# Kernel tuning notes

Measured on AMD Instinct MI355X. Metric: run time of the kernel, lower is better.

The kernel has to match this reference:

```python
import jax, jax.numpy as jnp
import numpy as np

SEQ, DIN, DOUT, RANK = 8192, 4096, 4096, 16

def setup_inputs() -> dict:
    key = jax.random.key(0)
    ks = jax.random.split(key, 5)
    return {
        "x": jax.random.normal(ks[0], (SEQ, DIN), dtype=jnp.float32),
        "W": jax.random.normal(ks[1], (DIN, DOUT), dtype=jnp.float32) * (1.0 / np.sqrt(DIN)),
        "bias": jax.random.normal(ks[2], (DOUT,), dtype=jnp.float32),
        "A_buffer": jax.random.normal(ks[3], (DIN, RANK), dtype=jnp.float32) * (1.0 / np.sqrt(DIN)),
        "B_buffer": jax.random.normal(ks[4], (RANK, DOUT), dtype=jnp.float32),
    }

def reference(x, W, bias, A_buffer, B_buffer):
    # base linear GEMM: [seq, in] @ [in, out] -> [seq, out]
    base_output = jnp.dot(x, W)
    # LoRA path: two low-rank GEMMs fused-added onto base output
    lora_a = jnp.dot(x, A_buffer)            # [seq, rank]
    output = base_output + jnp.dot(lora_a, B_buffer)  # [seq, out]
    # module returns (output, output_bias) with bias passed through separately
    return (output, bias)
```

## Files before the change

### kernel.cpp

```cpp
#include <hip/hip_runtime.h>
#include <cstdint>
#include <cstddef>


#define SEQ  8192
#define DIN  4096
#define DOUT 4096
#define RANK 16

typedef __attribute__((ext_vector_type(8))) __bf16 bf16x8;
typedef __attribute__((ext_vector_type(4))) float f32x4;
typedef __attribute__((ext_vector_type(8))) unsigned short ushort8;

#define CAST_BLOCKS ((SEQ * DIN) / (256 * 8))
#define WEFF_BLOCKS ((DOUT / 64) * (DIN / 64))

__device__ __forceinline__ unsigned short f32_to_bf16_rne(float f) {
  union { float f; unsigned int u; } cv;
  cv.f = f;
  unsigned int u = cv.u;
  u += 0x7FFFu + ((u >> 16) & 1u);
  return (unsigned short)(u >> 16);
}

__global__ __launch_bounds__(256) void cast_kernel(
    const float* __restrict__ x, unsigned short* __restrict__ xb,
    const float* __restrict__ bias, float* __restrict__ bias_out) {
  const int tid = blockIdx.x * 256 + threadIdx.x;
  const float4* x4 = (const float4*)x;
  float4 v0 = x4[(size_t)tid * 2 + 0];
  float4 v1 = x4[(size_t)tid * 2 + 1];
  ushort8 o;
  o[0] = f32_to_bf16_rne(v0.x); o[1] = f32_to_bf16_rne(v0.y);
  o[2] = f32_to_bf16_rne(v0.z); o[3] = f32_to_bf16_rne(v0.w);
  o[4] = f32_to_bf16_rne(v1.x); o[5] = f32_to_bf16_rne(v1.y);
  o[6] = f32_to_bf16_rne(v1.z); o[7] = f32_to_bf16_rne(v1.w);
  *(ushort8*)(xb + (size_t)tid * 8) = o;
  if (tid < DOUT) bias_out[tid] = bias[tid];
}

__global__ __launch_bounds__(256) void weff_kernel(
    const float* __restrict__ W, const float* __restrict__ A,
    const float* __restrict__ B, unsigned short* __restrict__ WT) {
  __shared__ float sBf[RANK][64];
  __shared__ float sAf[64][16];
  __shared__ unsigned short sT[64][65];
  const int blk = blockIdx.x;
  const int n0 = (blk & 63) * 64;
  const int k0 = (blk >> 6) * 64;
  const int t = threadIdx.x;

  #pragma unroll
  for (int pass = 0; pass < 4; ++pass) {
    const int idx = pass * 256 + t;
    sBf[idx >> 6][idx & 63] = B[(size_t)(idx >> 6) * DOUT + n0 + (idx & 63)];
    sAf[idx >> 4][idx & 15] = A[(size_t)(k0 + (idx >> 4)) * RANK + (idx & 15)];
  }
  __syncthreads();

  const int c   = t & 63;
  const int sub = t >> 6;
  float breg[16];
  #pragma unroll
  for (int r = 0; r < 16; ++r) breg[r] = sBf[r][c];

  #pragma unroll
  for (int p = 0; p < 16; ++p) {
    const int ki = p * 4 + sub;
    const float4* ar = (const float4*)sAf[ki];
    const float4 a0 = ar[0], a1 = ar[1], a2 = ar[2], a3 = ar[3];
    float acc = W[(size_t)(k0 + ki) * DOUT + n0 + c];
    acc += a0.x * breg[0]  + a0.y * breg[1]  + a0.z * breg[2]  + a0.w * breg[3];
    acc += a1.x * breg[4]  + a1.y * breg[5]  + a1.z * breg[6]  + a1.w * breg[7];
    acc += a2.x * breg[8]  + a2.y * breg[9]  + a2.z * breg[10] + a2.w * breg[11];
    acc += a3.x * breg[12] + a3.y * breg[13] + a3.z * breg[14] + a3.w * breg[15];
    sT[ki][c] = f32_to_bf16_rne(acc);
  }
  __syncthreads();

  #pragma unroll
  for (int s = 0; s < 2; ++s) {
    const int ni = (t >> 3) + s * 32;
    const int cc = t & 7;
    ushort8 o;
    #pragma unroll
    for (int u = 0; u < 8; ++u) o[u] = sT[cc * 8 + u][ni];
    *(ushort8*)(WT + (size_t)(n0 + ni) * DIN + k0 + cc * 8) = o;
  }
}

#define BM 256
#define BN 256
#define BK 64
#define GRID_X (DOUT / BN)
#define GRID_Y (SEQ / BM)
#define NWG (GRID_X * GRID_Y)

#define BARX()   asm volatile("s_barrier" ::: "memory")
#define LGKM(n)  asm volatile("s_waitcnt lgkmcnt(" #n ")" ::: "memory")
#define VMW(n)   asm volatile("s_waitcnt vmcnt(" #n ")" ::: "memory")

#define STAGE_AH(BUF, H, KOFF)                                                 \
  __builtin_amdgcn_global_load_lds(                                            \
      (const __attribute__((address_space(1))) void*)(gA + (size_t)((H)*128 + 0)  * DIN + (KOFF)),  \
      (__attribute__((address_space(3))) void*)(sA + (BUF)*16384 + (H)*8192 + 0    + t*8), 16, 0, 0);\
  __builtin_amdgcn_global_load_lds(                                            \
      (const __attribute__((address_space(1))) void*)(gA + (size_t)((H)*128 + 64) * DIN + (KOFF)),  \
      (__attribute__((address_space(3))) void*)(sA + (BUF)*16384 + (H)*8192 + 4096 + t*8), 16, 0, 0);

#define STAGE_BH(BUF, H, KOFF)                                                 \
  __builtin_amdgcn_global_load_lds(                                            \
      (const __attribute__((address_space(1))) void*)(gB + (size_t)((H)*128 + 0)  * DIN + (KOFF)),  \
      (__attribute__((address_space(3))) void*)(sB + (BUF)*16384 + (H)*8192 + 0    + t*8), 16, 0, 0);\
  __builtin_amdgcn_global_load_lds(                                            \
      (const __attribute__((address_space(1))) void*)(gB + (size_t)((H)*128 + 64) * DIN + (KOFF)),  \
      (__attribute__((address_space(3))) void*)(sB + (BUF)*16384 + (H)*8192 + 4096 + t*8), 16, 0, 0);

#define MFMA(A, B, C) __builtin_amdgcn_mfma_f32_16x16x32_bf16(A, B, C, 0, 0, 0)

#define KTILE(CUR, KOFF1, KOFF2, S1, S234, W1, W2, W4)                         \
  {                                                                            \
    const int ab_ = (CUR) * 16384;                                             \
    const int bb_ = (CUR) * 16384;                                             \
    bf16x8 a[4][2], b01[2][2], b23[2][2];                                      \
                                     \
    _Pragma("unroll") for (int i = 0; i < 4; ++i) {                            \
      a[i][0] = *(const bf16x8*)(sA + ab_ + aoff[i] + cp0);                    \
      a[i][1] = *(const bf16x8*)(sA + ab_ + aoff[i] + cp1); }                  \
    _Pragma("unroll") for (int j = 0; j < 2; ++j) {                            \
      b01[j][0] = *(const bf16x8*)(sB + bb_ + boff[j] + cp0);                  \
      b01[j][1] = *(const bf16x8*)(sB + bb_ + boff[j] + cp1); }                \
    if (S1) { STAGE_AH((CUR) ^ 1, 1, KOFF1); }                                 \
    LGKM(8);                                                                   \
    BARX(); LGKM(0);                                                           \
    __builtin_amdgcn_s_setprio(1);                                             \
    _Pragma("unroll") for (int i = 0; i < 4; ++i)                              \
      _Pragma("unroll") for (int j = 0; j < 2; ++j) {                          \
        acc[i][j] = MFMA(a[i][0], b01[j][0], acc[i][j]);                       \
        acc[i][j] = MFMA(a[i][1], b01[j][1], acc[i][j]); }                     \
    __builtin_amdgcn_s_setprio(0);                                             \
    VMW(W1); BARX();                                                           \
                                      \
    _Pragma("unroll") for (int j = 0; j < 2; ++j) {                            \
      b23[j][0] = *(const bf16x8*)(sB + bb_ + boff[j + 2] + cp0);              \
      b23[j][1] = *(const bf16x8*)(sB + bb_ + boff[j + 2] + cp1); }            \
    if (S234) { STAGE_BH((CUR), 0, KOFF2); }                                   \
    BARX(); LGKM(0);                                                           \
    __builtin_amdgcn_s_setprio(1);                                             \
    _Pragma("unroll") for (int i = 0; i < 4; ++i)                              \
      _Pragma("unroll") for (int j = 0; j < 2; ++j) {                          \
        acc[i][j + 2] = MFMA(a[i][0], b23[j][0], acc[i][j + 2]);               \
        acc[i][j + 2] = MFMA(a[i][1], b23[j][1], acc[i][j + 2]); }             \
    __builtin_amdgcn_s_setprio(0);                                             \
    VMW(W2); BARX();                                                           \
                                      \
    _Pragma("unroll") for (int i = 0; i < 4; ++i) {                            \
      a[i][0] = *(const bf16x8*)(sA + ab_ + aoff[i + 4] + cp0);                \
      a[i][1] = *(const bf16x8*)(sA + ab_ + aoff[i + 4] + cp1); }              \
    if (S234) { STAGE_AH((CUR), 0, KOFF2); }                                   \
    BARX(); LGKM(0);                                                           \
    __builtin_amdgcn_s_setprio(1);                                             \
    _Pragma("unroll") for (int i = 0; i < 4; ++i)                              \
      _Pragma("unroll") for (int j = 0; j < 2; ++j) {                          \
        acc[i + 4][j + 2] = MFMA(a[i][0], b23[j][0], acc[i + 4][j + 2]);       \
        acc[i + 4][j + 2] = MFMA(a[i][1], b23[j][1], acc[i + 4][j + 2]); }     \
    __builtin_amdgcn_s_setprio(0);                                             \
    BARX();                                                                    \
           \
    if (S234) { STAGE_BH((CUR), 1, KOFF2); }                                   \
    __builtin_amdgcn_s_setprio(1);                                             \
    _Pragma("unroll") for (int i = 0; i < 4; ++i)                              \
      _Pragma("unroll") for (int j = 0; j < 2; ++j) {                          \
        acc[i + 4][j] = MFMA(a[i][0], b01[j][0], acc[i + 4][j]);               \
        acc[i + 4][j] = MFMA(a[i][1], b01[j][1], acc[i + 4][j]); }             \
    __builtin_amdgcn_s_setprio(0);                                             \
    VMW(W4); BARX();                                                           \
  }

__global__ __launch_bounds__(512, 2) void gemm_bt_kernel(
    const unsigned short* __restrict__ xb, const unsigned short* __restrict__ wt,
    float* __restrict__ out) {
  __shared__ unsigned short sA[2 * BM * BK];
  __shared__ unsigned short sB[2 * BN * BK];

  const int t = threadIdx.x;
  const int lane = t & 63;
  const int w    = t >> 6;
  const int wr   = w >> 2;
  const int wc   = w & 3;
  const int quad = lane >> 4;
  const int lcol = lane & 15;

  const int lid = blockIdx.y * GRID_X + blockIdx.x;
  const int swz = (lid & 7) * (NWG / 8) + (lid >> 3);
  const int n0 = (swz & (GRID_X - 1)) * BN;
  const int m0 = (swz / GRID_X) * BM;

  const int g    = (lane & 7) ^ (lane >> 3);
  const int srow = w * 8 + (lane >> 3);
  const unsigned short* gA = xb + (size_t)(m0 + srow) * DIN + g * 8;
  const unsigned short* gB = wt + (size_t)(n0 + srow) * DIN + g * 8;

  const int xorv = lcol & 7;
  const int cp0  = (quad ^ xorv) * 8;
  const int cp1  = cp0 ^ 32;
  int aoff[8], boff[4];
  #pragma unroll
  for (int i = 0; i < 8; ++i)
    aoff[i] = ((i >> 2) * 128 + wr * 64 + (i & 3) * 16 + lcol) * 64;
  #pragma unroll
  for (int j = 0; j < 4; ++j)
    boff[j] = ((j >> 1) * 128 + wc * 32 + (j & 1) * 16 + lcol) * 64;

  f32x4 acc[8][4] = {};

  STAGE_AH(0, 0, 0);  STAGE_BH(0, 0, 0);  STAGE_BH(0, 1, 0);  STAGE_AH(0, 1, 0);
  STAGE_AH(1, 0, 64); STAGE_BH(1, 0, 64); STAGE_BH(1, 1, 64); STAGE_AH(1, 1, 64);
  VMW(12);
  BARX();

  KTILE(0, 64, 128, 0, 1, 10, 10, 10);

  #pragma unroll 2
  for (int tt = 1; tt < 62; ++tt) {
    const int cur = tt & 1;
    const int koff1 = (tt + 1) * BK;
    const int koff2 = (tt + 2) * BK;
    KTILE(cur, koff1, koff2, 1, 1, 10, 10, 10);
  }

  KTILE(0, 63 * BK, 0, 1, 0, 10, 8, 6);
  KTILE(1, 0, 0, 0, 0, 2, 0, 0);

  #pragma unroll
  for (int i = 0; i < 8; ++i) {
    const int rb = m0 + (i >> 2) * 128 + wr * 64 + (i & 3) * 16 + quad * 4;
    #pragma unroll
    for (int j = 0; j < 4; ++j) {
      const int cb = n0 + (j >> 1) * 128 + wc * 32 + (j & 1) * 16 + lcol;
      #pragma unroll
      for (int r = 0; r < 4; ++r)
        out[(size_t)(rb + r) * DOUT + cb] = acc[i][j][r];
    }
  }
}

extern "C" void kernel_launch(void* const* d_in, const int* in_sizes, int n_in,
                              void* d_out, int out_size, void* d_ws, size_t ws_size,
                              hipStream_t stream) {
  const float* x    = (const float*)d_in[0];
  const float* W    = (const float*)d_in[1];
  const float* bias = (const float*)d_in[2];
  const float* A    = (const float*)d_in[3];
  const float* B    = (const float*)d_in[4];
  float* out      = (float*)d_out;
  float* bias_out = out + (size_t)SEQ * DOUT;

  unsigned short* xb = (unsigned short*)d_ws;
  unsigned short* wt = xb + (size_t)SEQ * DIN;

  cast_kernel<<<CAST_BLOCKS, 256, 0, stream>>>(x, xb, bias, bias_out);
  weff_kernel<<<WEFF_BLOCKS, 256, 0, stream>>>(W, A, B, wt);
  gemm_bt_kernel<<<dim3(GRID_X, GRID_Y), 512, 0, stream>>>(xb, wt, out);
}
```

Measured before the change: 518.3 us.

## Restructure K-tile pipeline to drop barriers and LDS waitcnts, reorder staging

Reworks the per-K-tile schedule of the bf16 GEMM: removes the explicit lgkmcnt waits and one barrier per phase, moves the B-half-0 prefetch next to the A-half-0 prefetch, and passes per-phase vmcnt waits as macro arguments. The prologue now issues seven half-tile loads in B-first order and the loop starts at tile 0 instead of peeling it. The aim is fewer barrier stalls and better overlap of global-to-LDS loads with MFMA. Removing the lgkmcnt waits relies on the compiler inserting them for the LDS reads, and the changed vmcnt counts risk races if they are miscounted.

```diff
diff --git a/kernel.cpp b/kernel.cpp
--- a/kernel.cpp
+++ b/kernel.cpp
@@ -97,7 +97,6 @@
 #define NWG (GRID_X * GRID_Y)
 
 #define BARX()   asm volatile("s_barrier" ::: "memory")
-#define LGKM(n)  asm volatile("s_waitcnt lgkmcnt(" #n ")" ::: "memory")
 #define VMW(n)   asm volatile("s_waitcnt vmcnt(" #n ")" ::: "memory")
 
 #define STAGE_AH(BUF, H, KOFF)                                                 \
@@ -118,63 +117,57 @@
 
 #define MFMA(A, B, C) __builtin_amdgcn_mfma_f32_16x16x32_bf16(A, B, C, 0, 0, 0)
 
-#define KTILE(CUR, KOFF1, KOFF2, S1, S234, W1, W2, W4)                         \
+#define KTILE(CUR, KOFF1, KOFF2, S1, S34, W1, W2, W4)                          \
   {                                                                            \
     const int ab_ = (CUR) * 16384;                                             \
-    const int bb_ = (CUR) * 16384;                                             \
     bf16x8 a[4][2], b01[2][2], b23[2][2];                                      \
-                                     \
+                                                            \
     _Pragma("unroll") for (int i = 0; i < 4; ++i) {                            \
       a[i][0] = *(const bf16x8*)(sA + ab_ + aoff[i] + cp0);                    \
       a[i][1] = *(const bf16x8*)(sA + ab_ + aoff[i] + cp1); }                  \
     _Pragma("unroll") for (int j = 0; j < 2; ++j) {                            \
-      b01[j][0] = *(const bf16x8*)(sB + bb_ + boff[j] + cp0);                  \
-      b01[j][1] = *(const bf16x8*)(sB + bb_ + boff[j] + cp1); }                \
+      b01[j][0] = *(const bf16x8*)(sB + ab_ + boff[j] + cp0);                  \
+      b01[j][1] = *(const bf16x8*)(sB + ab_ + boff[j] + cp1); }                \
     if (S1) { STAGE_AH((CUR) ^ 1, 1, KOFF1); }                                 \
-    LGKM(8);                                                                   \
-    BARX(); LGKM(0);                                                           \
+    W1; BARX();                                                                \
     __builtin_amdgcn_s_setprio(1);                                             \
     _Pragma("unroll") for (int i = 0; i < 4; ++i)                              \
       _Pragma("unroll") for (int j = 0; j < 2; ++j) {                          \
         acc[i][j] = MFMA(a[i][0], b01[j][0], acc[i][j]);                       \
         acc[i][j] = MFMA(a[i][1], b01[j][1], acc[i][j]); }                     \
     __builtin_amdgcn_s_setprio(0);                                             \
-    VMW(W1); BARX();                                                           \
-                                      \
+                                                            \
     _Pragma("unroll") for (int j = 0; j < 2; ++j) {                            \
-      b23[j][0] = *(const bf16x8*)(sB + bb_ + boff[j + 2] + cp0);              \
-      b23[j][1] = *(const bf16x8*)(sB + bb_ + boff[j + 2] + cp1); }            \
-    if (S234) { STAGE_BH((CUR), 0, KOFF2); }                                   \
-    BARX(); LGKM(0);                                                           \
+      b23[j][0] = *(const bf16x8*)(sB + ab_ + boff[j + 2] + cp0);              \
+      b23[j][1] = *(const bf16x8*)(sB + ab_ + boff[j + 2] + cp1); }            \
+    W2; BARX();                                                                \
     __builtin_amdgcn_s_setprio(1);                                             \
     _Pragma("unroll") for (int i = 0; i < 4; ++i)                              \
       _Pragma("unroll") for (int j = 0; j < 2; ++j) {                          \
         acc[i][j + 2] = MFMA(a[i][0], b23[j][0], acc[i][j + 2]);               \
         acc[i][j + 2] = MFMA(a[i][1], b23[j][1], acc[i][j + 2]); }             \
     __builtin_amdgcn_s_setprio(0);                                             \
-    VMW(W2); BARX();                                                           \
-                                      \
+                                                            \
     _Pragma("unroll") for (int i = 0; i < 4; ++i) {                            \
       a[i][0] = *(const bf16x8*)(sA + ab_ + aoff[i + 4] + cp0);                \
       a[i][1] = *(const bf16x8*)(sA + ab_ + aoff[i + 4] + cp1); }              \
-    if (S234) { STAGE_AH((CUR), 0, KOFF2); }                                   \
-    BARX(); LGKM(0);                                                           \
+    if (S34) { STAGE_BH((CUR), 0, KOFF2); STAGE_AH((CUR), 0, KOFF2); }         \
+    BARX();                                                                    \
     __builtin_amdgcn_s_setprio(1);                                             \
     _Pragma("unroll") for (int i = 0; i < 4; ++i)                              \
       _Pragma("unroll") for (int j = 0; j < 2; ++j) {                          \
         acc[i + 4][j + 2] = MFMA(a[i][0], b23[j][0], acc[i + 4][j + 2]);       \
         acc[i + 4][j + 2] = MFMA(a[i][1], b23[j][1], acc[i + 4][j + 2]); }     \
     __builtin_amdgcn_s_setprio(0);                                             \
-    BARX();                                                                    \
-           \
-    if (S234) { STAGE_BH((CUR), 1, KOFF2); }                                   \
+                    \
+    if (S34) { STAGE_BH((CUR), 1, KOFF2); }                                    \
+    W4; BARX();                                                                \
     __builtin_amdgcn_s_setprio(1);                                             \
     _Pragma("unroll") for (int i = 0; i < 4; ++i)                              \
       _Pragma("unroll") for (int j = 0; j < 2; ++j) {                          \
         acc[i + 4][j] = MFMA(a[i][0], b01[j][0], acc[i + 4][j]);               \
         acc[i + 4][j] = MFMA(a[i][1], b01[j][1], acc[i + 4][j]); }             \
     __builtin_amdgcn_s_setprio(0);                                             \
-    VMW(W4); BARX();                                                           \
   }
 
 __global__ __launch_bounds__(512, 2) void gemm_bt_kernel(
@@ -214,23 +207,18 @@
 
   f32x4 acc[8][4] = {};
 
-  STAGE_AH(0, 0, 0);  STAGE_BH(0, 0, 0);  STAGE_BH(0, 1, 0);  STAGE_AH(0, 1, 0);
-  STAGE_AH(1, 0, 64); STAGE_BH(1, 0, 64); STAGE_BH(1, 1, 64); STAGE_AH(1, 1, 64);
-  VMW(12);
+  STAGE_BH(0, 0, 0);  STAGE_AH(0, 0, 0);  STAGE_BH(0, 1, 0);  STAGE_AH(0, 1, 0);
+  STAGE_BH(1, 0, 64); STAGE_AH(1, 0, 64); STAGE_BH(1, 1, 64);
+  VMW(10);
   BARX();
 
-  KTILE(0, 64, 128, 0, 1, 10, 10, 10);
-
   #pragma unroll 2
-  for (int tt = 1; tt < 62; ++tt) {
+  for (int tt = 0; tt < 62; ++tt) {
     const int cur = tt & 1;
-    const int koff1 = (tt + 1) * BK;
-    const int koff2 = (tt + 2) * BK;
-    KTILE(cur, koff1, koff2, 1, 1, 10, 10, 10);
-  }
-
-  KTILE(0, 63 * BK, 0, 1, 0, 10, 8, 6);
-  KTILE(1, 0, 0, 0, 0, 2, 0, 0);
+    KTILE(cur, (tt + 1) * BK, (tt + 2) * BK, 1, 1, VMW(10), VMW(8), VMW(10));
+  }
+  KTILE(0, 63 * BK, 0, 1, 0, VMW(10), VMW(8), VMW(4));
+  KTILE(1, 0, 0, 0, 0, VMW(2), VMW(0), ((void)0));
 
   #pragma unroll
   for (int i = 0; i < 8; ++i) {
```

Result: no change. 510.2 us (-1.6%).
